# Kernel optimization log

Hardware: AMD Instinct MI355X
Metric: run time of the kernel (lower is better)

The kernel has to match this reference:

```python
import jax, jax.numpy as jnp
import numpy as np

DIM, HID = 1024, 2048
N_SHARED, N_ROUTED, TOP_K = 2, 6, 2
AUX_W = 0.01
B, T = 4, 2048


def _swiglu(x, w1, w2, w3):
    # x: [N, C]; w1,w3: [C, H]; w2: [H, C]
    return (jax.nn.silu(x @ w1) * (x @ w3)) @ w2


def setup_inputs() -> dict:
    key = jax.random.key(0)
    ks = jax.random.split(key, 9)
    s = 0.02
    return {
        "x": jax.random.normal(ks[0], (B, T, DIM), dtype=jnp.float32),
        "w1_s": jax.random.normal(ks[1], (N_SHARED, DIM, HID), dtype=jnp.float32) * s,
        "w2_s": jax.random.normal(ks[2], (N_SHARED, HID, DIM), dtype=jnp.float32) * s,
        "w3_s": jax.random.normal(ks[3], (N_SHARED, DIM, HID), dtype=jnp.float32) * s,
        "w1_r": jax.random.normal(ks[4], (N_ROUTED, DIM, HID), dtype=jnp.float32) * s,
        "w2_r": jax.random.normal(ks[5], (N_ROUTED, HID, DIM), dtype=jnp.float32) * s,
        "w3_r": jax.random.normal(ks[6], (N_ROUTED, DIM, HID), dtype=jnp.float32) * s,
        "gate_w": jax.random.normal(ks[7], (DIM, N_ROUTED), dtype=jnp.float32) * s,
        "out_w": jax.random.normal(ks[8], (DIM, DIM), dtype=jnp.float32) * s,
    }


def reference(x, w1_s, w2_s, w3_s, w1_r, w2_r, w3_r, gate_w, out_w):
    Bv, Tv, C = x.shape
    xf = x.reshape(-1, C)  # [N, C]

    # shared experts: always run for every token
    shared = jnp.zeros_like(xf)
    for e in range(N_SHARED):
        shared = shared + _swiglu(xf, w1_s[e], w2_s[e], w3_s[e])

    # router
    logits = xf @ gate_w                       # [N, E]
    wk, idx = jax.lax.top_k(logits, TOP_K)     # [N, K]
    wk = jax.nn.softmax(wk, axis=-1)           # softmax over selected k only

    # routed experts: dense per-expert pass scaled by (zero for unselected) weight
    routed = jnp.zeros_like(xf)
    for e in range(N_ROUTED):
        we = jnp.sum(wk * (idx == e).astype(xf.dtype), axis=-1, keepdims=True)  # [N,1]
        routed = routed + we * _swiglu(xf, w1_r[e], w2_r[e], w3_r[e])

    combined = shared + routed

    # aux load-balance loss (top-1 assignment fraction x mean prob)
    probs = jax.nn.softmax(logits, axis=-1)
    f_i = jnp.mean(jax.nn.one_hot(idx[:, 0], N_ROUTED, dtype=xf.dtype), axis=0)
    p_i = jnp.mean(probs, axis=0)
    aux_loss = AUX_W * N_ROUTED * jnp.sum(f_i * p_i)

    out = (combined @ out_w).reshape(Bv, Tv, C)
    return out, aux_loss
```

## Files before the change

### kernel.cpp

```cpp
#include <hip/hip_runtime.h>
#include <hip/hip_bf16.h>
#include <cstdint>

#define DIMc 1024
#define HIDc 2048
#define NTOK 8192
#define NRT 6

typedef __bf16 bf16x8 __attribute__((ext_vector_type(8)));
typedef __bf16 bf16x2v __attribute__((ext_vector_type(2)));
typedef float  f32x4  __attribute__((ext_vector_type(4)));

#define VMCNT(n) asm volatile("s_waitcnt vmcnt(" #n ")" ::: "memory")
#define RBAR()   asm volatile("s_barrier" ::: "memory")

__device__ __forceinline__ void gl_lds16(const void* gsrc, void* ldst) {
    auto g = (const __attribute__((address_space(1))) void*)gsrc;
    auto l = (__attribute__((address_space(3))) void*)ldst;
    __builtin_amdgcn_global_load_lds(g, l, 16, 0, 0);
}

__device__ __forceinline__ void xcd_swz(int lid, int nwg, int gx, int& bx, int& by) {
    int q = nwg >> 3, r = nwg & 7;
    int xcd = lid & 7, idx = lid >> 3;
    int nlid = (xcd < r ? xcd * (q + 1) : r * (q + 1) + (xcd - r) * q) + idx;
    bx = nlid % gx; by = nlid / gx;
}

__global__ __launch_bounds__(256) void tcvt_k(
    const float* __restrict__ w1s, const float* __restrict__ w2s, const float* __restrict__ w3s,
    const float* __restrict__ w1r, const float* __restrict__ w2r, const float* __restrict__ w3r,
    const float* __restrict__ outw,
    __bf16* __restrict__ W13T, __bf16* __restrict__ W2T, __bf16* __restrict__ OutWT)
{
    int id = blockIdx.z;
    const float* src; __bf16* dst; int K, N; size_t S;
    if (id < 4) {
        int half = id >> 1, ex = id & 1;
        src = (half ? w3s : w1s) + (size_t)ex * DIMc * HIDc;
        K = 1024; N = 2048; S = 1024;
        dst = W13T + ((size_t)half * 4096 + ex * 2048) * 1024;
    } else if (id < 16) {
        int j = id - 4; int ex = j >> 1, half = j & 1;
        src = (half ? w3r : w1r) + (size_t)ex * DIMc * HIDc;
        K = 1024; N = 2048; S = 1024;
        dst = W13T + ((size_t)8192 + ex * 4096 + half * 2048) * 1024;
    } else if (id < 18) {
        int ex = id - 16;
        src = w2s + (size_t)ex * HIDc * DIMc;
        K = 2048; N = 1024; S = 4096;
        dst = W2T + ex * 2048;
    } else if (id < 24) {
        int ex = id - 18;
        src = w2r + (size_t)ex * HIDc * DIMc;
        K = 2048; N = 1024; S = 2048;
        dst = W2T + (size_t)4096 * 1024 + (size_t)ex * 2048 * 1024;
    } else {
        src = outw; K = 1024; N = 1024; S = 1024; dst = OutWT;
    }
    int n0 = blockIdx.x * 32, k0 = blockIdx.y * 32;
    if (n0 >= N || k0 >= K) return;
    __shared__ float t[32][33];
    int c = threadIdx.x & 31, rb = threadIdx.x >> 5;
#pragma unroll
    for (int i = 0; i < 4; i++) {
        int r = rb + i * 8;
        t[r][c] = src[(size_t)(k0 + r) * N + n0 + c];
    }
    __syncthreads();
    int kp = threadIdx.x & 15, nn = threadIdx.x >> 4;
#pragma unroll
    for (int pass = 0; pass < 2; pass++) {
        int n = nn + pass * 16;
        bf16x2v v; v[0] = (__bf16)t[2 * kp][n]; v[1] = (__bf16)t[2 * kp + 1][n];
        *(bf16x2v*)&dst[(size_t)(n0 + n) * S + k0 + 2 * kp] = v;
    }
}

__global__ __launch_bounds__(256) void router_k(
    const float* __restrict__ x, const float* __restrict__ gate,
    __bf16* __restrict__ xb, int* __restrict__ tke, float* __restrict__ tkw,
    float* __restrict__ auxp, float* __restrict__ auxf, int* __restrict__ rcnt)
{
    __shared__ float gl[DIMc * NRT];
    __shared__ float pacc[NRT];
    __shared__ int hist1[NRT], hist2[NRT];
    for (int i = threadIdx.x; i < DIMc * NRT; i += 256) gl[i] = gate[i];
    if (threadIdx.x < NRT) { pacc[threadIdx.x] = 0.f; hist1[threadIdx.x] = 0; hist2[threadIdx.x] = 0; }
    __syncthreads();
    int lane = threadIdx.x & 63, wid = threadIdx.x >> 6;
    for (int rep = 0; rep < 4; rep++) {
        int t = blockIdx.x * 16 + wid * 4 + rep;
        float a[NRT] = {0.f, 0.f, 0.f, 0.f, 0.f, 0.f};
        const float* xr = x + (size_t)t * DIMc;
        __bf16* xbr = xb + (size_t)t * DIMc;
        for (int k = lane; k < DIMc; k += 64) {
            float v = xr[k];
            xbr[k] = (__bf16)v;
#pragma unroll
            for (int e = 0; e < NRT; e++) a[e] += v * gl[k * NRT + e];
        }
#pragma unroll
        for (int e = 0; e < NRT; e++)
#pragma unroll
            for (int m = 32; m; m >>= 1) a[e] += __shfl_xor(a[e], m);
        if (lane == 0) {
            int i0 = 0; float m0 = a[0];
#pragma unroll
            for (int e = 1; e < NRT; e++) if (a[e] > m0) { m0 = a[e]; i0 = e; }
            int i1 = -1; float m1 = -1e30f;
#pragma unroll
            for (int e = 0; e < NRT; e++) if (e != i0 && a[e] > m1) { m1 = a[e]; i1 = e; }
            float w1 = __expf(m1 - m0);
            float inv = 1.f / (1.f + w1);
            tke[2 * t] = i0; tke[2 * t + 1] = i1;
            tkw[2 * t] = inv; tkw[2 * t + 1] = w1 * inv;
            float se = 0.f, pe[NRT];
#pragma unroll
            for (int e = 0; e < NRT; e++) { pe[e] = __expf(a[e] - m0); se += pe[e]; }
            float rinv = 1.f / se;
#pragma unroll
            for (int e = 0; e < NRT; e++) atomicAdd(&pacc[e], pe[e] * rinv);
            atomicAdd(&hist1[i0], 1);
            atomicAdd(&hist2[i0], 1); atomicAdd(&hist2[i1], 1);
        }
    }
    __syncthreads();
    if (threadIdx.x < NRT) {
        atomicAdd(&auxp[threadIdx.x], pacc[threadIdx.x]);
        atomicAdd(&auxf[threadIdx.x], (float)hist1[threadIdx.x]);
        atomicAdd(&rcnt[threadIdx.x], hist2[threadIdx.x]);
    }
}

__global__ void offsets_k(const int* __restrict__ rcnt, int* __restrict__ goff, int* __restrict__ gcnt) {
    if (threadIdx.x == 0) {
        int off = 0;
        for (int e = 0; e < NRT; e++) { goff[e] = off; gcnt[e] = rcnt[e]; off += rcnt[e]; }
    }
}

__global__ __launch_bounds__(256) void scatter_k(
    const int* __restrict__ tke, const float* __restrict__ tkw,
    const int* __restrict__ goff, int* __restrict__ curs,
    int* __restrict__ perm, float* __restrict__ wrow, int* __restrict__ islot)
{
    int t = blockIdx.x * 256 + threadIdx.x;
    if (t >= NTOK) return;
#pragma unroll
    for (int k = 0; k < 2; k++) {
        int e = tke[2 * t + k]; float w = tkw[2 * t + k];
        int slot = atomicAdd(&curs[e], 1);
        int sr = goff[e] + slot;
        perm[sr] = t; wrow[sr] = w; islot[2 * t + k] = sr;
    }
}

__global__ void auxfin_k(const float* __restrict__ auxp, const float* __restrict__ auxf, float* __restrict__ out) {
    if (threadIdx.x == 0) {
        float s = 0.f;
        for (int e = 0; e < NRT; e++) s += (auxf[e] * (1.f / NTOK)) * (auxp[e] * (1.f / NTOK));
        out[(size_t)NTOK * DIMc] = 0.01f * 6.f * s;
    }
}

template <int SHARED>
__global__ __launch_bounds__(512, 2) void gemm13_k(
    const __bf16* __restrict__ A, const __bf16* __restrict__ W13, __bf16* __restrict__ gbuf,
    const int* __restrict__ goff, const int* __restrict__ gcnt, const int* __restrict__ perm)
{
    __shared__ __bf16 lds[2 * 32768];
    int cnt, gofs, h3ofs, gstride;
    const __bf16* Bg;
    if constexpr (SHARED) {
        cnt = NTOK; gofs = 0; h3ofs = 4096 * 1024; gstride = 4096; Bg = W13;
    } else {
        int e = blockIdx.z;
        cnt = gcnt[e]; gofs = goff[e]; h3ofs = 2048 * 1024; gstride = 2048;
        Bg = W13 + ((size_t)8192 + (size_t)e * 4096) * 1024;
    }
    int bx, by;
    xcd_swz(blockIdx.x + gridDim.x * blockIdx.y, gridDim.x * gridDim.y, gridDim.x, bx, by);
    if (bx * 256 >= cnt) return;
    const int tid = threadIdx.x;
    const int lane = tid & 63, wid = tid >> 6;
    const int wr = wid >> 1, wc = wid & 1;
    const int l15 = lane & 15, l4 = lane >> 4;

    const __bf16* agA[4]; const __bf16* agB1[2]; const __bf16* agB3[2];
    int ldsA[4], ldsB[2];
#pragma unroll
    for (int i = 0; i < 4; i++) {
        int chunk = i * 512 + tid;
        int row = chunk >> 3, cg = (chunk & 7) ^ (row & 7);
        int r = bx * 256 + row; if (r > cnt - 1) r = cnt - 1;
        size_t arow = SHARED ? (size_t)r : (size_t)perm[gofs + r];
        agA[i] = A + arow * 1024 + cg * 8;
        ldsA[i] = chunk * 8;
    }
#pragma unroll
    for (int i = 0; i < 2; i++) {
        int chunk = i * 512 + tid;
        int row = chunk >> 3, cg = (chunk & 7) ^ (row & 7);
        int nr = by * 128 + row;
        agB1[i] = Bg + (size_t)nr * 1024 + cg * 8;
        agB3[i] = Bg + (size_t)h3ofs + (size_t)nr * 1024 + cg * 8;
        ldsB[i] = chunk * 8;
    }

#define STAGE13(b, kt) { __bf16* d_ = lds + (b) * 32768; \
    _Pragma("unroll") for (int i_ = 0; i_ < 4; i_++) gl_lds16(agA[i_] + (kt) * 64, d_ + ldsA[i_]); \
    _Pragma("unroll") for (int i_ = 0; i_ < 2; i_++) { \
        gl_lds16(agB1[i_] + (kt) * 64, d_ + 16384 + ldsB[i_]); \
        gl_lds16(agB3[i_] + (kt) * 64, d_ + 24576 + ldsB[i_]); } }

    f32x4 acc1[4][4], acc3[4][4];
#pragma unroll
    for (int mi = 0; mi < 4; mi++)
#pragma unroll
        for (int ni = 0; ni < 4; ni++)
#pragma unroll
            for (int j = 0; j < 4; j++) { acc1[mi][ni][j] = 0.f; acc3[mi][ni][j] = 0.f; }

    const int nkt = 16;
    STAGE13(0, 0);
    for (int kt = 0; kt < nkt; kt++) {
        const int cur = kt & 1;
        if (kt + 1 < nkt) { STAGE13(cur ^ 1, kt + 1); VMCNT(8); }
        else              { VMCNT(0); }
        RBAR();
        const __bf16* As  = lds + cur * 32768;
        const __bf16* B1s = As + 16384;
        const __bf16* B3s = As + 24576;
#pragma unroll
        for (int kk = 0; kk < 64; kk += 32) {
            bf16x8 av[4];
#pragma unroll
            for (int mi = 0; mi < 4; mi++) {
                int lr = wr * 64 + mi * 16 + l15;
                int cr = ((kk >> 3) + l4) ^ (lr & 7);
                av[mi] = *(const bf16x8*)&As[lr * 64 + cr * 8];
            }
#pragma unroll
            for (int ni = 0; ni < 4; ni++) {
                int lr = wc * 64 + ni * 16 + l15;
                int cr = ((kk >> 3) + l4) ^ (lr & 7);
                bf16x8 bv1 = *(const bf16x8*)&B1s[lr * 64 + cr * 8];
                bf16x8 bv3 = *(const bf16x8*)&B3s[lr * 64 + cr * 8];
#pragma unroll
                for (int mi = 0; mi < 4; mi++) {
                    acc1[mi][ni] = __builtin_amdgcn_mfma_f32_16x16x32_bf16(av[mi], bv1, acc1[mi][ni], 0, 0, 0);
                    acc3[mi][ni] = __builtin_amdgcn_mfma_f32_16x16x32_bf16(av[mi], bv3, acc3[mi][ni], 0, 0, 0);
                }
            }
        }
        RBAR();
    }

#pragma unroll
    for (int mi = 0; mi < 4; mi++) {
#pragma unroll
        for (int j = 0; j < 4; j++) {
            int r = bx * 256 + wr * 64 + mi * 16 + l4 * 4 + j;
            if (r < cnt) {
                size_t orow = (size_t)(gofs + r) * gstride;
#pragma unroll
                for (int ni = 0; ni < 4; ni++) {
                    int c = by * 128 + wc * 64 + ni * 16 + l15;
                    float h1 = acc1[mi][ni][j], h3 = acc3[mi][ni][j];
                    float sg = h1 / (1.f + __expf(-h1));
                    gbuf[orow + c] = (__bf16)(sg * h3);
                }
            }
        }
    }
#undef STAGE13
}

template <int MODE>
__global__ __launch_bounds__(256, 2) void gemmNN_k(
    const __bf16* __restrict__ A, const __bf16* __restrict__ B,
    __bf16* __restrict__ outB16, float* __restrict__ outF32,
    const float* __restrict__ wrow, const int* __restrict__ goff, const int* __restrict__ gcnt,
    int K)
{
    __shared__ __bf16 lds[2 * 16384];
    int cnt, gofs;
    const __bf16* Bg;
    if constexpr (MODE == 1) {
        int e = blockIdx.z;
        cnt = gcnt[e]; gofs = goff[e];
        Bg = B + (size_t)e * 2048 * 1024;
    } else {
        cnt = NTOK; gofs = 0; Bg = B;
    }
    int bx, by;
    xcd_swz(blockIdx.x + gridDim.x * blockIdx.y, gridDim.x * gridDim.y, gridDim.x, bx, by);
    if (bx * 128 >= cnt) return;
    const int tid = threadIdx.x;
    const int lane = tid & 63, wid = tid >> 6;
    const int wr = wid >> 1, wc = wid & 1;
    const int l15 = lane & 15, l4 = lane >> 4;

    const __bf16* agA[4]; const __bf16* agB[4];
    int ldsOf[4];
#pragma unroll
    for (int i = 0; i < 4; i++) {
        int chunk = i * 256 + tid;
        int row = chunk >> 3, cg = (chunk & 7) ^ (row & 7);
        int r = bx * 128 + row; if (r > cnt - 1) r = cnt - 1;
        agA[i] = A + (size_t)(gofs + r) * K + cg * 8;
        agB[i] = Bg + (size_t)(by * 128 + row) * K + cg * 8;
        ldsOf[i] = chunk * 8;
    }

#define STAGENN(b, kt) { __bf16* d_ = lds + (b) * 16384; \
    _Pragma("unroll") for (int i_ = 0; i_ < 4; i_++) { \
        gl_lds16(agA[i_] + (kt) * 64, d_ + ldsOf[i_]); \
        gl_lds16(agB[i_] + (kt) * 64, d_ + 8192 + ldsOf[i_]); } }

    f32x4 acc[4][4];
#pragma unroll
    for (int mi = 0; mi < 4; mi++)
#pragma unroll
        for (int ni = 0; ni < 4; ni++)
#pragma unroll
            for (int j = 0; j < 4; j++) acc[mi][ni][j] = 0.f;

    const int nkt = K >> 6;
    STAGENN(0, 0);
    for (int kt = 0; kt < nkt; kt++) {
        const int cur = kt & 1;
        if (kt + 1 < nkt) { STAGENN(cur ^ 1, kt + 1); VMCNT(8); }
        else              { VMCNT(0); }
        RBAR();
        const __bf16* As = lds + cur * 16384;
        const __bf16* Bs = As + 8192;
#pragma unroll
        for (int kk = 0; kk < 64; kk += 32) {
            bf16x8 av[4];
#pragma unroll
            for (int mi = 0; mi < 4; mi++) {
                int lr = wr * 64 + mi * 16 + l15;
                int cr = ((kk >> 3) + l4) ^ (lr & 7);
                av[mi] = *(const bf16x8*)&As[lr * 64 + cr * 8];
            }
#pragma unroll
            for (int ni = 0; ni < 4; ni++) {
                int lr = wc * 64 + ni * 16 + l15;
                int cr = ((kk >> 3) + l4) ^ (lr & 7);
                bf16x8 bv = *(const bf16x8*)&Bs[lr * 64 + cr * 8];
#pragma unroll
                for (int mi = 0; mi < 4; mi++)
                    acc[mi][ni] = __builtin_amdgcn_mfma_f32_16x16x32_bf16(av[mi], bv, acc[mi][ni], 0, 0, 0);
            }
        }
        RBAR();
    }

#pragma unroll
    for (int mi = 0; mi < 4; mi++) {
#pragma unroll
        for (int j = 0; j < 4; j++) {
            int r = bx * 128 + wr * 64 + mi * 16 + l4 * 4 + j;
            if (r < cnt) {
                if constexpr (MODE == 0) {
                    size_t orow = (size_t)r * 1024;
#pragma unroll
                    for (int ni = 0; ni < 4; ni++) {
                        int c = by * 128 + wc * 64 + ni * 16 + l15;
                        outB16[orow + c] = (__bf16)acc[mi][ni][j];
                    }
                } else if constexpr (MODE == 1) {
                    int sr = gofs + r;
                    float w = wrow[sr];
                    size_t orow = (size_t)(8192 + sr) * 1024;
#pragma unroll
                    for (int ni = 0; ni < 4; ni++) {
                        int c = by * 128 + wc * 64 + ni * 16 + l15;
                        outB16[orow + c] = (__bf16)(w * acc[mi][ni][j]);
                    }
                } else {
                    size_t orow = (size_t)r * 1024;
#pragma unroll
                    for (int ni = 0; ni < 4; ni++) {
                        int c = by * 128 + wc * 64 + ni * 16 + l15;
                        outF32[orow + c] = acc[mi][ni][j];
                    }
                }
            }
        }
    }
#undef STAGENN
}

__global__ __launch_bounds__(256) void combine_k(
    const __bf16* __restrict__ ybuf, const int* __restrict__ islot, __bf16* __restrict__ cb)
{
    int tid = threadIdx.x;
    int row = blockIdx.x * 2 + (tid >> 7);
    int c8 = (tid & 127) * 8;
    int s0 = islot[2 * row], s1 = islot[2 * row + 1];
    bf16x8 vs = *(const bf16x8*)&ybuf[(size_t)row * 1024 + c8];
    bf16x8 v0 = *(const bf16x8*)&ybuf[(size_t)(8192 + s0) * 1024 + c8];
    bf16x8 v1 = *(const bf16x8*)&ybuf[(size_t)(8192 + s1) * 1024 + c8];
    bf16x8 o;
#pragma unroll
    for (int j = 0; j < 8; j++) o[j] = (__bf16)((float)vs[j] + (float)v0[j] + (float)v1[j]);
    *(bf16x8*)&cb[(size_t)row * 1024 + c8] = o;
}

extern "C" void kernel_launch(void* const* d_in, const int* in_sizes, int n_in,
                              void* d_out, int out_size, void* d_ws, size_t ws_size,
                              hipStream_t stream) {
    const float* x    = (const float*)d_in[0];
    const float* w1s  = (const float*)d_in[1];
    const float* w2s  = (const float*)d_in[2];
    const float* w3s  = (const float*)d_in[3];
    const float* w1r  = (const float*)d_in[4];
    const float* w2r  = (const float*)d_in[5];
    const float* w3r  = (const float*)d_in[6];
    const float* gate = (const float*)d_in[7];
    const float* outw = (const float*)d_in[8];
    float* out = (float*)d_out;

    char* ws = (char*)d_ws;
    float* auxp = (float*)ws;
    float* auxf = auxp + 8;
    int*   rcnt = (int*)(ws + 64);
    int*   curs = rcnt + 8;
    size_t off = 256;
    __bf16* xb    = (__bf16*)(ws + off); off += 16777216;
    __bf16* W13T  = (__bf16*)(ws + off); off += 67108864;
    __bf16* W2T   = (__bf16*)(ws + off); off += 33554432;
    __bf16* OutWT = (__bf16*)(ws + off); off += 2097152;
    __bf16* gbuf  = (__bf16*)(ws + off); off += 67108864;
    __bf16* cb    = gbuf;
    __bf16* ybuf  = (__bf16*)(ws + off); off += 50331648;
    int*   tke   = (int*)(ws + off);   off += 65536;
    float* tkw   = (float*)(ws + off); off += 65536;
    int*   perm  = (int*)(ws + off);   off += 65536;
    float* wrow  = (float*)(ws + off); off += 65536;
    int*   islot = (int*)(ws + off);   off += 65536;
    int*   goffp = (int*)(ws + off);   off += 64;
    int*   gcntp = (int*)(ws + off);   off += 64;

    hipMemsetAsync(d_ws, 0, 256, stream);

    dim3 b256(256), b512(512);
    tcvt_k<<<dim3(64, 64, 25), b256, 0, stream>>>(w1s, w2s, w3s, w1r, w2r, w3r, outw, W13T, W2T, OutWT);
    router_k<<<dim3(512), b256, 0, stream>>>(x, gate, xb, tke, tkw, auxp, auxf, rcnt);
    offsets_k<<<dim3(1), dim3(64), 0, stream>>>(rcnt, goffp, gcntp);
    scatter_k<<<dim3(32), b256, 0, stream>>>(tke, tkw, goffp, curs, perm, wrow, islot);
    auxfin_k<<<dim3(1), dim3(64), 0, stream>>>(auxp, auxf, out);

    gemm13_k<1><<<dim3(32, 32, 1), b512, 0, stream>>>(xb, W13T, gbuf, goffp, gcntp, perm);
    gemmNN_k<0><<<dim3(64, 8, 1), b256, 0, stream>>>(gbuf, W2T, ybuf, nullptr, wrow, goffp, gcntp, 4096);
    gemm13_k<0><<<dim3(32, 16, 6), b512, 0, stream>>>(xb, W13T, gbuf, goffp, gcntp, perm);
    gemmNN_k<1><<<dim3(64, 8, 6), b256, 0, stream>>>(gbuf, W2T + (size_t)4096 * 1024, ybuf, nullptr, wrow, goffp, gcntp, 2048);

    combine_k<<<dim3(4096), b256, 0, stream>>>(ybuf, islot, cb);
    gemmNN_k<2><<<dim3(64, 8, 1), b256, 0, stream>>>(cb, OutWT, nullptr, out, wrow, goffp, gcntp, 1024);
}
```

Before: 865.1 us.

## Use 4-stage K=32 LDS pipeline and larger 512-thread tiles in MoE GEMMs

Both the fused W1/W3 GEMM and the down/output GEMMs move from a double-buffered K=64 loop to a four-slot ring of K=32 stages. Loads are issued three tiles ahead, with graded vmcnt waits and a single barrier per step, and MFMA blocks are wrapped in s_setprio. The W1/W3 kernel interleaves w1 and w3 rows in 16-row groups so one B tile feeds a single accumulator array. gemmNN grows to 512 threads with 256-row tiles, and its grids are resized to match. The XOR swizzle on LDS is dropped in favour of plain 64-byte rows, which risks LDS bank conflicts; the larger LDS footprint may also limit occupancy.

After: 924.4 us. 6.9% more time.

```diff
diff --git a/kernel.cpp b/kernel.cpp
--- a/kernel.cpp
+++ b/kernel.cpp
@@ -169,14 +169,14 @@
     const __bf16* __restrict__ A, const __bf16* __restrict__ W13, __bf16* __restrict__ gbuf,
     const int* __restrict__ goff, const int* __restrict__ gcnt, const int* __restrict__ perm)
 {
-    __shared__ __bf16 lds[2 * 32768];
-    int cnt, gofs, h3ofs, gstride;
+    __shared__ __bf16 lds[4 * 16384];
+    int cnt, gofs, h3row, gstride;
     const __bf16* Bg;
     if constexpr (SHARED) {
-        cnt = NTOK; gofs = 0; h3ofs = 4096 * 1024; gstride = 4096; Bg = W13;
+        cnt = NTOK; gofs = 0; h3row = 4096; gstride = 4096; Bg = W13;
     } else {
         int e = blockIdx.z;
-        cnt = gcnt[e]; gofs = goff[e]; h3ofs = 2048 * 1024; gstride = 2048;
+        cnt = gcnt[e]; gofs = goff[e]; h3row = 2048; gstride = 2048;
         Bg = W13 + ((size_t)8192 + (size_t)e * 4096) * 1024;
     }
     int bx, by;
@@ -184,107 +184,97 @@
     if (bx * 256 >= cnt) return;
     const int tid = threadIdx.x;
     const int lane = tid & 63, wid = tid >> 6;
-    const int wr = wid >> 1, wc = wid & 1;
+    const int wr = wid >> 2, wc = wid & 3;
     const int l15 = lane & 15, l4 = lane >> 4;
 
-    const __bf16* agA[4]; const __bf16* agB1[2]; const __bf16* agB3[2];
-    int ldsA[4], ldsB[2];
-#pragma unroll
-    for (int i = 0; i < 4; i++) {
-        int chunk = i * 512 + tid;
-        int row = chunk >> 3, cg = (chunk & 7) ^ (row & 7);
-        int r = bx * 256 + row; if (r > cnt - 1) r = cnt - 1;
+    const __bf16* agA[2]; const __bf16* agB[2];
+    int ldsA[2], ldsB[2];
+#pragma unroll
+    for (int i = 0; i < 2; i++) {
+        int cA = i * 512 + tid;
+        int rowA = cA >> 2, qA = cA & 3;
+        int r = bx * 256 + rowA; if (r > cnt - 1) r = cnt - 1;
         size_t arow = SHARED ? (size_t)r : (size_t)perm[gofs + r];
-        agA[i] = A + arow * 1024 + cg * 8;
-        ldsA[i] = chunk * 8;
-    }
-#pragma unroll
-    for (int i = 0; i < 2; i++) {
-        int chunk = i * 512 + tid;
-        int row = chunk >> 3, cg = (chunk & 7) ^ (row & 7);
-        int nr = by * 128 + row;
-        agB1[i] = Bg + (size_t)nr * 1024 + cg * 8;
-        agB3[i] = Bg + (size_t)h3ofs + (size_t)nr * 1024 + cg * 8;
-        ldsB[i] = chunk * 8;
-    }
-
-#define STAGE13(b, kt) { __bf16* d_ = lds + (b) * 32768; \
-    _Pragma("unroll") for (int i_ = 0; i_ < 4; i_++) gl_lds16(agA[i_] + (kt) * 64, d_ + ldsA[i_]); \
-    _Pragma("unroll") for (int i_ = 0; i_ < 2; i_++) { \
-        gl_lds16(agB1[i_] + (kt) * 64, d_ + 16384 + ldsB[i_]); \
-        gl_lds16(agB3[i_] + (kt) * 64, d_ + 24576 + ldsB[i_]); } }
-
-    f32x4 acc1[4][4], acc3[4][4];
-#pragma unroll
-    for (int mi = 0; mi < 4; mi++)
+        agA[i] = A + arow * 1024 + qA * 8;
+        ldsA[i] = cA * 8;
+        int cB = i * 512 + tid;
+        int jr = cB >> 2, qB = cB & 3;
+        int g = jr >> 5, s = jr & 31;
+        int r1 = by * 128 + g * 16 + (s & 15);
+        int brow = (s < 16) ? r1 : (h3row + r1);
+        agB[i] = Bg + (size_t)brow * 1024 + qB * 8;
+        ldsB[i] = cB * 8;
+    }
+
+#define STG13(slot, kt) { __bf16* d_ = lds + (slot) * 16384; \
+    gl_lds16(agA[0] + (kt) * 32, d_ + ldsA[0]); \
+    gl_lds16(agA[1] + (kt) * 32, d_ + ldsA[1]); \
+    gl_lds16(agB[0] + (kt) * 32, d_ + 8192 + ldsB[0]); \
+    gl_lds16(agB[1] + (kt) * 32, d_ + 8192 + ldsB[1]); }
+
+    f32x4 acc[8][4];
+#pragma unroll
+    for (int mi = 0; mi < 8; mi++)
 #pragma unroll
         for (int ni = 0; ni < 4; ni++)
 #pragma unroll
-            for (int j = 0; j < 4; j++) { acc1[mi][ni][j] = 0.f; acc3[mi][ni][j] = 0.f; }
-
-    const int nkt = 16;
-    STAGE13(0, 0);
-    for (int kt = 0; kt < nkt; kt++) {
-        const int cur = kt & 1;
-        if (kt + 1 < nkt) { STAGE13(cur ^ 1, kt + 1); VMCNT(8); }
-        else              { VMCNT(0); }
-        RBAR();
-        const __bf16* As  = lds + cur * 32768;
-        const __bf16* B1s = As + 16384;
-        const __bf16* B3s = As + 24576;
-#pragma unroll
-        for (int kk = 0; kk < 64; kk += 32) {
-            bf16x8 av[4];
-#pragma unroll
-            for (int mi = 0; mi < 4; mi++) {
-                int lr = wr * 64 + mi * 16 + l15;
-                int cr = ((kk >> 3) + l4) ^ (lr & 7);
-                av[mi] = *(const bf16x8*)&As[lr * 64 + cr * 8];
-            }
-#pragma unroll
-            for (int ni = 0; ni < 4; ni++) {
-                int lr = wc * 64 + ni * 16 + l15;
-                int cr = ((kk >> 3) + l4) ^ (lr & 7);
-                bf16x8 bv1 = *(const bf16x8*)&B1s[lr * 64 + cr * 8];
-                bf16x8 bv3 = *(const bf16x8*)&B3s[lr * 64 + cr * 8];
-#pragma unroll
-                for (int mi = 0; mi < 4; mi++) {
-                    acc1[mi][ni] = __builtin_amdgcn_mfma_f32_16x16x32_bf16(av[mi], bv1, acc1[mi][ni], 0, 0, 0);
-                    acc3[mi][ni] = __builtin_amdgcn_mfma_f32_16x16x32_bf16(av[mi], bv3, acc3[mi][ni], 0, 0, 0);
-                }
-            }
-        }
-        RBAR();
-    }
-
-#pragma unroll
-    for (int mi = 0; mi < 4; mi++) {
+            for (int j = 0; j < 4; j++) acc[mi][ni][j] = 0.f;
+
+#define CMP13(slot) { \
+    const __bf16* As = lds + (slot) * 16384; \
+    const __bf16* Bs = As + 8192; \
+    bf16x8 av[8], bv[4]; \
+    _Pragma("unroll") for (int mi = 0; mi < 8; mi++) \
+        av[mi] = *(const bf16x8*)&As[(wr * 128 + mi * 16 + l15) * 32 + l4 * 8]; \
+    _Pragma("unroll") for (int ni = 0; ni < 4; ni++) \
+        bv[ni] = *(const bf16x8*)&Bs[(wc * 64 + ni * 16 + l15) * 32 + l4 * 8]; \
+    __builtin_amdgcn_s_setprio(1); \
+    _Pragma("unroll") for (int mi = 0; mi < 8; mi++) \
+        _Pragma("unroll") for (int ni = 0; ni < 4; ni++) \
+            acc[mi][ni] = __builtin_amdgcn_mfma_f32_16x16x32_bf16(av[mi], bv[ni], acc[mi][ni], 0, 0, 0); \
+    __builtin_amdgcn_s_setprio(0); }
+
+    const int nkt = 32;
+    STG13(0, 0); STG13(1, 1); STG13(2, 2);
+    int kt = 0;
+    for (; kt < nkt - 3; kt++) {
+        VMCNT(8); RBAR();
+        STG13((kt + 3) & 3, kt + 3);
+        CMP13(kt & 3);
+    }
+    VMCNT(8); RBAR(); CMP13(kt & 3); kt++;
+    VMCNT(4); RBAR(); CMP13(kt & 3); kt++;
+    VMCNT(0); RBAR(); CMP13(kt & 3);
+
+#pragma unroll
+    for (int mi = 0; mi < 8; mi++) {
 #pragma unroll
         for (int j = 0; j < 4; j++) {
-            int r = bx * 256 + wr * 64 + mi * 16 + l4 * 4 + j;
+            int r = bx * 256 + wr * 128 + mi * 16 + l4 * 4 + j;
             if (r < cnt) {
                 size_t orow = (size_t)(gofs + r) * gstride;
 #pragma unroll
-                for (int ni = 0; ni < 4; ni++) {
-                    int c = by * 128 + wc * 64 + ni * 16 + l15;
-                    float h1 = acc1[mi][ni][j], h3 = acc3[mi][ni][j];
+                for (int p = 0; p < 2; p++) {
+                    int c = by * 128 + wc * 32 + p * 16 + l15;
+                    float h1 = acc[mi][2 * p][j], h3 = acc[mi][2 * p + 1][j];
                     float sg = h1 / (1.f + __expf(-h1));
                     gbuf[orow + c] = (__bf16)(sg * h3);
                 }
             }
         }
     }
-#undef STAGE13
+#undef STG13
+#undef CMP13
 }
 
 template <int MODE>
-__global__ __launch_bounds__(256, 2) void gemmNN_k(
+__global__ __launch_bounds__(512, 2) void gemmNN_k(
     const __bf16* __restrict__ A, const __bf16* __restrict__ B,
     __bf16* __restrict__ outB16, float* __restrict__ outF32,
     const float* __restrict__ wrow, const int* __restrict__ goff, const int* __restrict__ gcnt,
     int K)
 {
-    __shared__ __bf16 lds[2 * 16384];
+    __shared__ __bf16 lds[4 * 12288];
     int cnt, gofs;
     const __bf16* Bg;
     if constexpr (MODE == 1) {
@@ -296,28 +286,33 @@
     }
     int bx, by;
     xcd_swz(blockIdx.x + gridDim.x * blockIdx.y, gridDim.x * gridDim.y, gridDim.x, bx, by);
-    if (bx * 128 >= cnt) return;
+    if (bx * 256 >= cnt) return;
     const int tid = threadIdx.x;
     const int lane = tid & 63, wid = tid >> 6;
     const int wr = wid >> 1, wc = wid & 1;
     const int l15 = lane & 15, l4 = lane >> 4;
 
-    const __bf16* agA[4]; const __bf16* agB[4];
-    int ldsOf[4];
-#pragma unroll
-    for (int i = 0; i < 4; i++) {
-        int chunk = i * 256 + tid;
-        int row = chunk >> 3, cg = (chunk & 7) ^ (row & 7);
-        int r = bx * 128 + row; if (r > cnt - 1) r = cnt - 1;
-        agA[i] = A + (size_t)(gofs + r) * K + cg * 8;
-        agB[i] = Bg + (size_t)(by * 128 + row) * K + cg * 8;
-        ldsOf[i] = chunk * 8;
-    }
-
-#define STAGENN(b, kt) { __bf16* d_ = lds + (b) * 16384; \
-    _Pragma("unroll") for (int i_ = 0; i_ < 4; i_++) { \
-        gl_lds16(agA[i_] + (kt) * 64, d_ + ldsOf[i_]); \
-        gl_lds16(agB[i_] + (kt) * 64, d_ + 8192 + ldsOf[i_]); } }
+    const __bf16* agA[2]; const __bf16* agB1;
+    int ldsA[2], ldsB1;
+#pragma unroll
+    for (int i = 0; i < 2; i++) {
+        int cA = i * 512 + tid;
+        int rowA = cA >> 2, qA = cA & 3;
+        int r = bx * 256 + rowA; if (r > cnt - 1) r = cnt - 1;
+        agA[i] = A + (size_t)(gofs + r) * K + qA * 8;
+        ldsA[i] = cA * 8;
+    }
+    {
+        int cB = tid;
+        int jr = cB >> 2, qB = cB & 3;
+        agB1 = Bg + (size_t)(by * 128 + jr) * K + qB * 8;
+        ldsB1 = cB * 8;
+    }
+
+#define STGNN(slot, kt) { __bf16* d_ = lds + (slot) * 12288; \
+    gl_lds16(agA[0] + (kt) * 32, d_ + ldsA[0]); \
+    gl_lds16(agA[1] + (kt) * 32, d_ + ldsA[1]); \
+    gl_lds16(agB1 + (kt) * 32, d_ + 8192 + ldsB1); }
 
     f32x4 acc[4][4];
 #pragma unroll
@@ -327,42 +322,37 @@
 #pragma unroll
             for (int j = 0; j < 4; j++) acc[mi][ni][j] = 0.f;
 
-    const int nkt = K >> 6;
-    STAGENN(0, 0);
-    for (int kt = 0; kt < nkt; kt++) {
-        const int cur = kt & 1;
-        if (kt + 1 < nkt) { STAGENN(cur ^ 1, kt + 1); VMCNT(8); }
-        else              { VMCNT(0); }
-        RBAR();
-        const __bf16* As = lds + cur * 16384;
-        const __bf16* Bs = As + 8192;
-#pragma unroll
-        for (int kk = 0; kk < 64; kk += 32) {
-            bf16x8 av[4];
-#pragma unroll
-            for (int mi = 0; mi < 4; mi++) {
-                int lr = wr * 64 + mi * 16 + l15;
-                int cr = ((kk >> 3) + l4) ^ (lr & 7);
-                av[mi] = *(const bf16x8*)&As[lr * 64 + cr * 8];
-            }
-#pragma unroll
-            for (int ni = 0; ni < 4; ni++) {
-                int lr = wc * 64 + ni * 16 + l15;
-                int cr = ((kk >> 3) + l4) ^ (lr & 7);
-                bf16x8 bv = *(const bf16x8*)&Bs[lr * 64 + cr * 8];
-#pragma unroll
-                for (int mi = 0; mi < 4; mi++)
-                    acc[mi][ni] = __builtin_amdgcn_mfma_f32_16x16x32_bf16(av[mi], bv, acc[mi][ni], 0, 0, 0);
-            }
-        }
-        RBAR();
-    }
+#define CMPNN(slot) { \
+    const __bf16* As = lds + (slot) * 12288; \
+    const __bf16* Bs = As + 8192; \
+    bf16x8 av[4], bv[4]; \
+    _Pragma("unroll") for (int mi = 0; mi < 4; mi++) \
+        av[mi] = *(const bf16x8*)&As[(wr * 64 + mi * 16 + l15) * 32 + l4 * 8]; \
+    _Pragma("unroll") for (int ni = 0; ni < 4; ni++) \
+        bv[ni] = *(const bf16x8*)&Bs[(wc * 64 + ni * 16 + l15) * 32 + l4 * 8]; \
+    __builtin_amdgcn_s_setprio(1); \
+    _Pragma("unroll") for (int mi = 0; mi < 4; mi++) \
+        _Pragma("unroll") for (int ni = 0; ni < 4; ni++) \
+            acc[mi][ni] = __builtin_amdgcn_mfma_f32_16x16x32_bf16(av[mi], bv[ni], acc[mi][ni], 0, 0, 0); \
+    __builtin_amdgcn_s_setprio(0); }
+
+    const int nkt = K >> 5;
+    STGNN(0, 0); STGNN(1, 1); STGNN(2, 2);
+    int kt = 0;
+    for (; kt < nkt - 3; kt++) {
+        VMCNT(6); RBAR();
+        STGNN((kt + 3) & 3, kt + 3);
+        CMPNN(kt & 3);
+    }
+    VMCNT(6); RBAR(); CMPNN(kt & 3); kt++;
+    VMCNT(3); RBAR(); CMPNN(kt & 3); kt++;
+    VMCNT(0); RBAR(); CMPNN(kt & 3);
 
 #pragma unroll
     for (int mi = 0; mi < 4; mi++) {
 #pragma unroll
         for (int j = 0; j < 4; j++) {
-            int r = bx * 128 + wr * 64 + mi * 16 + l4 * 4 + j;
+            int r = bx * 256 + wr * 64 + mi * 16 + l4 * 4 + j;
             if (r < cnt) {
                 if constexpr (MODE == 0) {
                     size_t orow = (size_t)r * 1024;
@@ -391,7 +381,8 @@
             }
         }
     }
-#undef STAGENN
+#undef STGNN
+#undef CMPNN
 }
 
 __global__ __launch_bounds__(256) void combine_k(
@@ -455,10 +446,10 @@
     auxfin_k<<<dim3(1), dim3(64), 0, stream>>>(auxp, auxf, out);
 
     gemm13_k<1><<<dim3(32, 32, 1), b512, 0, stream>>>(xb, W13T, gbuf, goffp, gcntp, perm);
-    gemmNN_k<0><<<dim3(64, 8, 1), b256, 0, stream>>>(gbuf, W2T, ybuf, nullptr, wrow, goffp, gcntp, 4096);
+    gemmNN_k<0><<<dim3(32, 8, 1), b512, 0, stream>>>(gbuf, W2T, ybuf, nullptr, wrow, goffp, gcntp, 4096);
     gemm13_k<0><<<dim3(32, 16, 6), b512, 0, stream>>>(xb, W13T, gbuf, goffp, gcntp, perm);
-    gemmNN_k<1><<<dim3(64, 8, 6), b256, 0, stream>>>(gbuf, W2T + (size_t)4096 * 1024, ybuf, nullptr, wrow, goffp, gcntp, 2048);
+    gemmNN_k<1><<<dim3(64, 8, 6), b512, 0, stream>>>(gbuf, W2T + (size_t)4096 * 1024, ybuf, nullptr, wrow, goffp, gcntp, 2048);
 
     combine_k<<<dim3(4096), b256, 0, stream>>>(ybuf, islot, cb);
-    gemmNN_k<2><<<dim3(64, 8, 1), b256, 0, stream>>>(cb, OutWT, nullptr, out, wrow, goffp, gcntp, 1024);
-}
+    gemmNN_k<2><<<dim3(32, 8, 1), b512, 0, stream>>>(cb, OutWT, nullptr, out, wrow, goffp, gcntp, 1024);
+}
```
